# Kernel optimization log

Measured on AMD Instinct MI355X. Metric: run time of the kernel, lower is better.

The kernel has to match this reference:

```python
import jax, jax.numpy as jnp
import numpy as np

C = 64        # in_channels
E = 64        # embed_dim
K_RATIO = 0.5


def _conv(x, w, b, pad, groups):
    # x: [B,C,H,W], w: [O, I/groups, kh, kw] (torch OIHW layout)
    y = jax.lax.conv_general_dilated(
        x, w, window_strides=(1, 1), padding=[(pad, pad), (pad, pad)],
        dimension_numbers=("NCHW", "OIHW", "NCHW"), feature_group_count=groups)
    return y + b[None, :, None, None]


def setup_inputs() -> dict:
    key = jax.random.key(0)
    ks = jax.random.split(key, 16)
    s = 0.05
    return {
        "x": jax.random.normal(ks[0], (8, C, 64, 64), jnp.float32),
        "w1": jax.random.normal(ks[1], (C, C, 1, 1), jnp.float32) * s,
        "b1": jax.random.normal(ks[2], (C,), jnp.float32) * s,
        "w3": jax.random.normal(ks[3], (C, 1, 3, 3), jnp.float32) * s,
        "b3": jax.random.normal(ks[4], (C,), jnp.float32) * s,
        "w5": jax.random.normal(ks[5], (C, 1, 5, 5), jnp.float32) * s,
        "b5": jax.random.normal(ks[6], (C,), jnp.float32) * s,
        "qw": jax.random.normal(ks[7], (E, 3 * C), jnp.float32) * s,
        "qb": jax.random.normal(ks[8], (E,), jnp.float32) * s,
        "kw": jax.random.normal(ks[9], (E, 3 * C), jnp.float32) * s,
        "kb": jax.random.normal(ks[10], (E,), jnp.float32) * s,
        "vw": jax.random.normal(ks[11], (C, 3 * C), jnp.float32) * s,
        "vb": jax.random.normal(ks[12], (C,), jnp.float32) * s,
        "ow": jax.random.normal(ks[13], (C, C), jnp.float32) * s,
        "ob": jax.random.normal(ks[14], (C,), jnp.float32) * s,
    }


def reference(x, w1, b1, w3, b3, w5, b5, qw, qb, kw, kb, vw, vb, ow, ob):
    b, c, h, w = x.shape
    N = h * w
    f1 = _conv(x, w1, b1, pad=0, groups=1)        # 1x1 conv
    f2 = _conv(x, w3, b3, pad=1, groups=c)        # 3x3 depthwise
    f3 = _conv(x, w5, b5, pad=2, groups=c)        # 5x5 depthwise
    f_multi = jnp.concatenate([f1, f2, f3], axis=1)           # [b, 3c, h, w]
    f_flat = f_multi.reshape(b, 3 * c, N).transpose(0, 2, 1)  # [b, N, 3c]

    Q = jnp.einsum("bnd,ed->bne", f_flat, qw) + qb            # [b, N, E]
    K = jnp.einsum("bnd,ed->bne", f_flat, kw) + kb            # [b, N, E]
    V = jnp.einsum("bnd,cd->bnc", f_flat, vw) + vb            # [b, N, c]

    attn = jnp.einsum("bqe,bke->bqk", Q, K) / jnp.sqrt(jnp.float32(E))
    attn = jax.nn.softmax(attn, axis=-1)                      # [b, N, N]

    key_importance = attn.sum(axis=1)                         # [b, N]
    k_val = max(1, min(int(N * K_RATIO), N))
    _, topk_idx = jax.lax.top_k(key_importance, k_val)        # [b, k_val]
    mask = jnp.zeros_like(key_importance).at[
        jnp.arange(b)[:, None], topk_idx].set(1.0)            # [b, N]

    attn_c = attn * mask[:, None, :]
    attn_c = attn_c / (attn_c.sum(axis=-1, keepdims=True) + 1e-8)
    out = jnp.einsum("bqk,bkc->bqc", attn_c, V)               # [b, N, c]
    out = jnp.einsum("bnc,oc->bno", out, ow) + ob
    return out.transpose(0, 2, 1).reshape(b, c, h, w)
```

## Files before the change

kernel.cpp:

```cpp
#include <hip/hip_runtime.h>
#include <hip/hip_bf16.h>

typedef unsigned short ushort;
typedef __bf16 bf16x8 __attribute__((ext_vector_type(8)));
typedef float f32x4 __attribute__((ext_vector_type(4)));

__device__ __forceinline__ ushort f2bu(float f) {
  __hip_bfloat16 h = __float2bfloat16(f);
  return *(ushort*)&h;
}
__device__ __forceinline__ f32x4 mfma16(bf16x8 a, bf16x8 b, f32x4 c) {
  return __builtin_amdgcn_mfma_f32_16x16x32_bf16(a, b, c, 0, 0, 0);
}


__global__ __launch_bounds__(256) void k_conv(
    const float* __restrict__ x, const float* __restrict__ w1, const float* __restrict__ b1,
    const float* __restrict__ w3, const float* __restrict__ b3,
    const float* __restrict__ w5, const float* __restrict__ b5,
    ushort* __restrict__ f) {
  __shared__ float xs[64][64];
  __shared__ float w1s[64 * 65];
  __shared__ float w3s[576];
  __shared__ float w5s[1600];
  __shared__ float bs1[64], bs3[64], bs5[64];
  const int tid = threadIdx.x;
  const int y = blockIdx.x;
  const int b = blockIdx.y;
  for (int i = tid; i < 4096; i += 256) {
    int ch = i >> 6, w = i & 63;
    xs[ch][w] = x[((size_t)(b * 64 + ch) * 64 + y) * 64 + w];
  }
  for (int i = tid; i < 4096; i += 256) w1s[(i >> 6) * 65 + (i & 63)] = w1[i];
  for (int i = tid; i < 576; i += 256) w3s[i] = w3[i];
  for (int i = tid; i < 1600; i += 256) w5s[i] = w5[i];
  if (tid < 64) { bs1[tid] = b1[tid]; bs3[tid] = b3[tid]; bs5[tid] = b5[tid]; }
  __syncthreads();
  const int px = tid & 63;
  const int cg = tid >> 6;
  const int cb = cg * 16;
  ushort* fo = f + ((size_t)b * 4096 + y * 64 + px) * 192;
  float a1[16];
#pragma unroll
  for (int j = 0; j < 16; j++) a1[j] = bs1[cb + j];
  for (int ic = 0; ic < 64; ic++) {
    float xv = xs[ic][px];
#pragma unroll
    for (int j = 0; j < 16; j++) a1[j] += w1s[(cb + j) * 65 + ic] * xv;
  }
#pragma unroll
  for (int j = 0; j < 16; j++) fo[cb + j] = f2bu(a1[j]);
#pragma unroll 4
  for (int j = 0; j < 16; j++) {
    int c = cb + j;
    const float* xc = x + (size_t)(b * 64 + c) * 4096;
    float a3 = bs3[c], a5 = bs5[c];
#pragma unroll
    for (int dy = 0; dy < 5; dy++) {
      int yy = y + dy - 2;
      if (yy < 0 || yy >= 64) continue;
      const float* xr = xc + yy * 64;
#pragma unroll
      for (int dx = 0; dx < 5; dx++) {
        int wx = px + dx - 2;
        float v = (wx >= 0 && wx < 64) ? xr[wx] : 0.f;
        a5 += w5s[c * 25 + dy * 5 + dx] * v;
        if (dy >= 1 && dy <= 3 && dx >= 1 && dx <= 3)
          a3 += w3s[c * 9 + (dy - 1) * 3 + (dx - 1)] * v;
      }
    }
    fo[64 + c] = f2bu(a3);
    fo[128 + c] = f2bu(a5);
  }
}

__global__ __launch_bounds__(256) void k_w2b(
    const float* __restrict__ qw, const float* __restrict__ kw,
    const float* __restrict__ vw, ushort* __restrict__ Wb) {
  int i = blockIdx.x * 256 + threadIdx.x;
  const float* src = (i < 12288) ? qw : (i < 24576) ? kw : vw;
  int off = (i < 12288) ? i : (i < 24576) ? (i - 12288) : (i - 24576);
  Wb[i] = f2bu(src[off]);
}

__global__ __launch_bounds__(256) void k_qkv(
    const ushort* __restrict__ F, const ushort* __restrict__ Wb,
    const float* __restrict__ qb, const float* __restrict__ kb,
    const float* __restrict__ vb,
    ushort* __restrict__ Q, ushort* __restrict__ K, ushort* __restrict__ V) {
  __shared__ __align__(16) ushort fs[64][200];
  const int tid = threadIdx.x;
  const int w = tid >> 6;
  const int lane = tid & 63;
  const int col = lane & 15;
  const int quad = lane >> 4;
  const size_t rowbase = (size_t)blockIdx.x * 64;
  for (int i = tid; i < 1536; i += 256) {
    int r = i / 24, c8 = i % 24;
    *(uint4*)&fs[r][c8 * 8] = *(const uint4*)&F[rowbase * 192 + (size_t)i * 8];
  }
  __syncthreads();
  bf16x8 af[6];
#pragma unroll
  for (int kk = 0; kk < 6; kk++)
    af[kk] = *(const bf16x8*)&fs[w * 16 + col][kk * 32 + quad * 8];
  ushort* const outp[3] = {Q, K, V};
  const float* const bp[3] = {qb, kb, vb};
#pragma unroll
  for (int sel = 0; sel < 3; sel++) {
    const ushort* wsel = Wb + sel * 12288;
    const float sc = (sel == 0) ? 0.125f : 1.0f;
#pragma unroll
    for (int ntl = 0; ntl < 4; ntl++) {
      const ushort* brow = wsel + (ntl * 16 + col) * 192 + quad * 8;
      f32x4 acc = {0.f, 0.f, 0.f, 0.f};
#pragma unroll
      for (int kk = 0; kk < 6; kk++) {
        bf16x8 bf = *(const bf16x8*)&brow[kk * 32];
        acc = mfma16(af[kk], bf, acc);
      }
      float bv = bp[sel][ntl * 16 + col];
#pragma unroll
      for (int r = 0; r < 4; r++)
        outp[sel][(rowbase + w * 16 + quad * 4 + r) * 64 + ntl * 16 + col] =
            f2bu((acc[r] + bv) * sc);
    }
  }
}

__global__ __launch_bounds__(256) void k_sumexp(
    const ushort* __restrict__ Qb, const ushort* __restrict__ Kb,
    float* __restrict__ Lo, float* __restrict__ IP) {
  __shared__ float red[4][64];
  __shared__ float lred[64];
  const int tid = threadIdx.x;
  const int b = blockIdx.x & 7;
  const int qt = blockIdx.x >> 3;
  const int lane = tid & 63;
  const int w = tid >> 6;
  const int col = lane & 15;
  const int quad = lane >> 4;
  const size_t qbase = (size_t)b * 4096 + qt * 64;
  const size_t kbase = (size_t)b * 4096;
  bf16x8 af[4][2];
#pragma unroll
  for (int t = 0; t < 4; t++)
#pragma unroll
    for (int h = 0; h < 2; h++)
      af[t][h] = *(const bf16x8*)&Qb[(qbase + t * 16 + col) * 64 + quad * 8 + h * 32];
  const ushort* kp = &Kb[(kbase + w * 16 + col) * 64 + quad * 8];
  float lacc[4][4];
#pragma unroll
  for (int t = 0; t < 4; t++)
#pragma unroll
    for (int r = 0; r < 4; r++) lacc[t][r] = 0.f;
  bf16x8 nb0 = *(const bf16x8*)kp;
  bf16x8 nb1 = *(const bf16x8*)(kp + 32);
  for (int kt = 0; kt < 64; kt++) {
    bf16x8 b0 = nb0, b1 = nb1;
    if (kt < 63) {
      nb0 = *(const bf16x8*)(kp + (size_t)(kt + 1) * 4096);
      nb1 = *(const bf16x8*)(kp + (size_t)(kt + 1) * 4096 + 32);
    }
#pragma unroll
    for (int t = 0; t < 4; t++) {
      f32x4 acc = {0.f, 0.f, 0.f, 0.f};
      acc = mfma16(af[t][0], b0, acc);
      acc = mfma16(af[t][1], b1, acc);
#pragma unroll
      for (int r = 0; r < 4; r++) lacc[t][r] += __expf(acc[r]);
    }
  }
#pragma unroll
  for (int t = 0; t < 4; t++)
#pragma unroll
    for (int r = 0; r < 4; r++) {
      float v = lacc[t][r];
      v += __shfl_xor(v, 1); v += __shfl_xor(v, 2);
      v += __shfl_xor(v, 4); v += __shfl_xor(v, 8);
      if (col == 0) red[w][t * 16 + quad * 4 + r] = v;
    }
  __syncthreads();
  if (tid < 64) {
    float l = red[0][tid] + red[1][tid] + red[2][tid] + red[3][tid];
    Lo[qbase + tid] = l;
    lred[tid] = 1.f / l;
  }
  __syncthreads();
  float linv[4][4];
#pragma unroll
  for (int t = 0; t < 4; t++)
#pragma unroll
    for (int r = 0; r < 4; r++) linv[t][r] = lred[t * 16 + quad * 4 + r];
  nb0 = *(const bf16x8*)kp;
  nb1 = *(const bf16x8*)(kp + 32);
  for (int kt = 0; kt < 64; kt++) {
    bf16x8 b0 = nb0, b1 = nb1;
    if (kt < 63) {
      nb0 = *(const bf16x8*)(kp + (size_t)(kt + 1) * 4096);
      nb1 = *(const bf16x8*)(kp + (size_t)(kt + 1) * 4096 + 32);
    }
    float ip = 0.f;
#pragma unroll
    for (int t = 0; t < 4; t++) {
      f32x4 acc = {0.f, 0.f, 0.f, 0.f};
      acc = mfma16(af[t][0], b0, acc);
      acc = mfma16(af[t][1], b1, acc);
#pragma unroll
      for (int r = 0; r < 4; r++) ip += __expf(acc[r]) * linv[t][r];
    }
    ip += __shfl_xor(ip, 16);
    ip += __shfl_xor(ip, 32);
    if (quad == 0)
      IP[((size_t)(b * 64 + qt)) * 4096 + kt * 64 + w * 16 + col] = ip;
  }
}

__global__ __launch_bounds__(256) void k_impsum(
    const float* __restrict__ IP, float* __restrict__ imp) {
  const int tid = threadIdx.x;
  const int b = blockIdx.y;
  const int col = blockIdx.x * 256 + tid;
  const float* p = IP + (size_t)b * 64 * 4096 + col;
  float s = 0.f;
#pragma unroll 8
  for (int r = 0; r < 64; r++) s += p[(size_t)r * 4096];
  imp[(size_t)b * 4096 + col] = s;
}

__global__ __launch_bounds__(256) void k_mask2c(
    const float* __restrict__ imp, const ushort* __restrict__ Kb,
    const ushort* __restrict__ Vb, ushort* __restrict__ Kc,
    ushort* __restrict__ Vc) {
  __shared__ __align__(16) float imps[4096];
  __shared__ int part[4][64];
  const int tid = threadIdx.x;
  const int b = blockIdx.y;
  const int base = blockIdx.x * 64;
  for (int i = tid; i < 4096; i += 256) imps[i] = imp[(size_t)b * 4096 + i];
  __syncthreads();
  const int cand = tid & 63;
  const int seg = tid >> 6;
  const int k = base + cand;
  const float v = imps[k];
  int cnt = 0;
  const int j0 = seg * 1024;
  for (int j = j0; j < j0 + 1024; j += 4) {
    float4 a = *(const float4*)&imps[j];
    cnt += (a.x > v) ? 1 : ((a.x == v && (j + 0) < k) ? 1 : 0);
    cnt += (a.y > v) ? 1 : ((a.y == v && (j + 1) < k) ? 1 : 0);
    cnt += (a.z > v) ? 1 : ((a.z == v && (j + 2) < k) ? 1 : 0);
    cnt += (a.w > v) ? 1 : ((a.w == v && (j + 3) < k) ? 1 : 0);
  }
  part[seg][cand] = cnt;
  __syncthreads();
  const int c = part[0][cand] + part[1][cand] + part[2][cand] + part[3][cand];
  if (c < 2048) {
    const ushort* ksrc = &Kb[((size_t)b * 4096 + k) * 64 + seg * 16];
    const ushort* vsrc = &Vb[((size_t)b * 4096 + k) * 64 + seg * 16];
    ushort* kdst = &Kc[((size_t)b * 2048 + c) * 64 + seg * 16];
    ushort* vdst = &Vc[((size_t)b * 2048 + c) * 64 + seg * 16];
    *(uint4*)kdst = *(const uint4*)ksrc;
    *(uint4*)(kdst + 8) = *(const uint4*)(ksrc + 8);
    *(uint4*)vdst = *(const uint4*)vsrc;
    *(uint4*)(vdst + 8) = *(const uint4*)(vsrc + 8);
  }
}

__global__ __launch_bounds__(256) void k_attn_out(
    const ushort* __restrict__ Qb, const ushort* __restrict__ Kc,
    const ushort* __restrict__ Vc, const float* __restrict__ Lo,
    const float* __restrict__ owp, const float* __restrict__ obp,
    float* __restrict__ out) {
  __shared__ __align__(16) ushort Vt[64][72];
  __shared__ __align__(16) ushort Ps[64][72];
  __shared__ __align__(16) ushort ows[64][72];
  __shared__ float dred[4][64];
  __shared__ float lqs[64];
  const int tid = threadIdx.x;
  const int b = blockIdx.x & 7;
  const int qt = blockIdx.x >> 3;
  const int lane = tid & 63;
  const int w = tid >> 6;
  const int col = lane & 15;
  const int quad = lane >> 4;
  const size_t qbase = (size_t)b * 4096 + qt * 64;
  const size_t kbase = (size_t)b * 2048;
  bf16x8 af[4][2];
#pragma unroll
  for (int t = 0; t < 4; t++)
#pragma unroll
    for (int h = 0; h < 2; h++)
      af[t][h] = *(const bf16x8*)&Qb[(qbase + t * 16 + col) * 64 + quad * 8 + h * 32];
  for (int i = tid; i < 4096; i += 256) ows[i >> 6][i & 63] = f2bu(owp[i]);
  if (tid < 64) lqs[tid] = Lo[qbase + tid];
  f32x4 pv[4];
  float dpacc[4][4];
#pragma unroll
  for (int t = 0; t < 4; t++) {
    pv[t] = (f32x4){0.f, 0.f, 0.f, 0.f};
#pragma unroll
    for (int r = 0; r < 4; r++) dpacc[t][r] = 0.f;
  }
  const int vrow = tid & 63;
  const int vch = tid >> 6;
  const ushort* kp = &Kc[(kbase + w * 16 + col) * 64 + quad * 8];
  bf16x8 nb0 = *(const bf16x8*)kp;
  bf16x8 nb1 = *(const bf16x8*)(kp + 32);
  for (int kt = 0; kt < 32; kt++) {
    __syncthreads();
    {
      const ushort* vsrc = &Vc[(kbase + kt * 64 + vrow) * 64 + vch * 16];
      uint4 v0 = *(const uint4*)vsrc;
      uint4 v1 = *(const uint4*)(vsrc + 8);
      ushort tmp[16];
      *(uint4*)&tmp[0] = v0;
      *(uint4*)&tmp[8] = v1;
#pragma unroll
      for (int j = 0; j < 16; j++) Vt[vch * 16 + j][vrow] = tmp[j];
    }
    bf16x8 b0 = nb0, b1 = nb1;
    if (kt < 31) {
      nb0 = *(const bf16x8*)(kp + (size_t)(kt + 1) * 4096);
      nb1 = *(const bf16x8*)(kp + (size_t)(kt + 1) * 4096 + 32);
    }
#pragma unroll
    for (int t = 0; t < 4; t++) {
      f32x4 acc = {0.f, 0.f, 0.f, 0.f};
      acc = mfma16(af[t][0], b0, acc);
      acc = mfma16(af[t][1], b1, acc);
#pragma unroll
      for (int r = 0; r < 4; r++) {
        float p = __expf(acc[r]);
        dpacc[t][r] += p;
        Ps[t * 16 + quad * 4 + r][w * 16 + col] = f2bu(p);
      }
    }
    __syncthreads();
    bf16x8 v0f = *(const bf16x8*)&Vt[w * 16 + col][quad * 8];
    bf16x8 v1f = *(const bf16x8*)&Vt[w * 16 + col][quad * 8 + 32];
#pragma unroll
    for (int t = 0; t < 4; t++) {
      bf16x8 p0 = *(const bf16x8*)&Ps[t * 16 + col][quad * 8];
      bf16x8 p1 = *(const bf16x8*)&Ps[t * 16 + col][quad * 8 + 32];
      pv[t] = mfma16(p0, v0f, pv[t]);
      pv[t] = mfma16(p1, v1f, pv[t]);
    }
  }
#pragma unroll
  for (int t = 0; t < 4; t++)
#pragma unroll
    for (int r = 0; r < 4; r++) {
      float v = dpacc[t][r];
      v += __shfl_xor(v, 1); v += __shfl_xor(v, 2);
      v += __shfl_xor(v, 4); v += __shfl_xor(v, 8);
      if (col == 0) dred[w][t * 16 + quad * 4 + r] = v;
    }
  __syncthreads();
#pragma unroll
  for (int t = 0; t < 4; t++)
#pragma unroll
    for (int r = 0; r < 4; r++) {
      int q = t * 16 + quad * 4 + r;
      float den = dred[0][q] + dred[1][q] + dred[2][q] + dred[3][q] + 1e-8f * lqs[q];
      Ps[q][w * 16 + col] = f2bu(pv[t][r] / den);
    }
  __syncthreads();
  bf16x8 w0 = *(const bf16x8*)&ows[w * 16 + col][quad * 8];
  bf16x8 w1 = *(const bf16x8*)&ows[w * 16 + col][quad * 8 + 32];
  const float obv = obp[w * 16 + col];
#pragma unroll
  for (int t = 0; t < 4; t++) {
    bf16x8 p0 = *(const bf16x8*)&Ps[t * 16 + col][quad * 8];
    bf16x8 p1 = *(const bf16x8*)&Ps[t * 16 + col][quad * 8 + 32];
    f32x4 oc = {0.f, 0.f, 0.f, 0.f};
    oc = mfma16(p0, w0, oc);
    oc = mfma16(p1, w1, oc);
#pragma unroll
    for (int r = 0; r < 4; r++) {
      int q = t * 16 + quad * 4 + r;
      int co = w * 16 + col;
      out[((size_t)(b * 64 + co)) * 4096 + qt * 64 + q] = oc[r] + obv;
    }
  }
}

extern "C" void kernel_launch(void* const* d_in, const int* in_sizes, int n_in,
                              void* d_out, int out_size, void* d_ws, size_t ws_size,
                              hipStream_t stream) {
  const float* x  = (const float*)d_in[0];
  const float* w1 = (const float*)d_in[1];
  const float* b1 = (const float*)d_in[2];
  const float* w3 = (const float*)d_in[3];
  const float* b3 = (const float*)d_in[4];
  const float* w5 = (const float*)d_in[5];
  const float* b5 = (const float*)d_in[6];
  const float* qw = (const float*)d_in[7];
  const float* qb = (const float*)d_in[8];
  const float* kw = (const float*)d_in[9];
  const float* kb = (const float*)d_in[10];
  const float* vw = (const float*)d_in[11];
  const float* vb = (const float*)d_in[12];
  const float* ow = (const float*)d_in[13];
  const float* ob = (const float*)d_in[14];
  float* out = (float*)d_out;
  float* ws = (float*)d_ws;
  ushort* F   = (ushort*)ws;
  ushort* Qb  = (ushort*)(ws + 6291456);
  ushort* Kb  = (ushort*)(ws + 7340032);
  ushort* Vb  = (ushort*)(ws + 8388608);
  float*  Lo  = ws + 9437184;
  float*  IP  = ws + 9469952;
  float*  imp = ws + 11567104;
  ushort* Kc  = (ushort*)(ws + 11599872);
  ushort* Vc  = (ushort*)(ws + 12124160);
  ushort* Wb  = (ushort*)(ws + 12648448);

  k_w2b<<<144, 256, 0, stream>>>(qw, kw, vw, Wb);
  k_conv<<<dim3(64, 8), 256, 0, stream>>>(x, w1, b1, w3, b3, w5, b5, F);
  k_qkv<<<512, 256, 0, stream>>>(F, Wb, qb, kb, vb, Qb, Kb, Vb);
  k_sumexp<<<512, 256, 0, stream>>>(Qb, Kb, Lo, IP);
  k_impsum<<<dim3(16, 8), 256, 0, stream>>>(IP, imp);
  k_mask2c<<<dim3(64, 8), 256, 0, stream>>>(imp, Kb, Vb, Kc, Vc);
  k_attn_out<<<512, 256, 0, stream>>>(Qb, Kc, Vc, Lo, ow, ob, out);
}
```

Measured before the change: 327.0 us.

## Split sumexp over key halves into separate kernels and use exp2 with prescaled Q

The fused sumexp kernel becomes two kernels, each split across two key halves. That doubles the grid to 1024 blocks for more parallelism on the many CUs, and a small combine kernel merges the partial row sums and their reciprocals. Q is now prescaled by log2(e), so every exponential uses the hardware exp2 instead of __expf. The cost is two extra launches and a global round trip for the partial sums. The workspace offsets are also compacted.

```diff
diff --git a/kernel.cpp b/kernel.cpp
--- a/kernel.cpp
+++ b/kernel.cpp
@@ -12,6 +12,7 @@
 __device__ __forceinline__ f32x4 mfma16(bf16x8 a, bf16x8 b, f32x4 c) {
   return __builtin_amdgcn_mfma_f32_16x16x32_bf16(a, b, c, 0, 0, 0);
 }
+__device__ __forceinline__ float fexp2(float x) { return __builtin_amdgcn_exp2f(x); }
 
 
 __global__ __launch_bounds__(256) void k_conv(
@@ -109,7 +110,7 @@
 #pragma unroll
   for (int sel = 0; sel < 3; sel++) {
     const ushort* wsel = Wb + sel * 12288;
-    const float sc = (sel == 0) ? 0.125f : 1.0f;
+    const float sc = (sel == 0) ? 0.125f * 1.44269504088896f : 1.0f;
 #pragma unroll
     for (int ntl = 0; ntl < 4; ntl++) {
       const ushort* brow = wsel + (ntl * 16 + col) * 192 + quad * 8;
@@ -128,20 +129,21 @@
   }
 }
 
-__global__ __launch_bounds__(256) void k_sumexp(
+__global__ __launch_bounds__(256) void k_sumexp_l(
     const ushort* __restrict__ Qb, const ushort* __restrict__ Kb,
-    float* __restrict__ Lo, float* __restrict__ IP) {
+    float* __restrict__ Lp) {
   __shared__ float red[4][64];
-  __shared__ float lred[64];
   const int tid = threadIdx.x;
   const int b = blockIdx.x & 7;
-  const int qt = blockIdx.x >> 3;
+  const int rest = blockIdx.x >> 3;
+  const int qt = rest & 63;
+  const int kh = rest >> 6;
   const int lane = tid & 63;
   const int w = tid >> 6;
   const int col = lane & 15;
   const int quad = lane >> 4;
   const size_t qbase = (size_t)b * 4096 + qt * 64;
-  const size_t kbase = (size_t)b * 4096;
+  const size_t kbase = (size_t)b * 4096 + kh * 2048;
   bf16x8 af[4][2];
 #pragma unroll
   for (int t = 0; t < 4; t++)
@@ -156,9 +158,9 @@
     for (int r = 0; r < 4; r++) lacc[t][r] = 0.f;
   bf16x8 nb0 = *(const bf16x8*)kp;
   bf16x8 nb1 = *(const bf16x8*)(kp + 32);
-  for (int kt = 0; kt < 64; kt++) {
+  for (int kt = 0; kt < 32; kt++) {
     bf16x8 b0 = nb0, b1 = nb1;
-    if (kt < 63) {
+    if (kt < 31) {
       nb0 = *(const bf16x8*)(kp + (size_t)(kt + 1) * 4096);
       nb1 = *(const bf16x8*)(kp + (size_t)(kt + 1) * 4096 + 32);
     }
@@ -168,7 +170,7 @@
       acc = mfma16(af[t][0], b0, acc);
       acc = mfma16(af[t][1], b1, acc);
 #pragma unroll
-      for (int r = 0; r < 4; r++) lacc[t][r] += __expf(acc[r]);
+      for (int r = 0; r < 4; r++) lacc[t][r] += fexp2(acc[r]);
     }
   }
 #pragma unroll
@@ -183,20 +185,53 @@
   __syncthreads();
   if (tid < 64) {
     float l = red[0][tid] + red[1][tid] + red[2][tid] + red[3][tid];
-    Lo[qbase + tid] = l;
-    lred[tid] = 1.f / l;
-  }
+    Lp[((size_t)(b * 64 + qt) * 2 + kh) * 64 + tid] = l;
+  }
+}
+
+__global__ __launch_bounds__(256) void k_lcomb(
+    const float* __restrict__ Lp, float* __restrict__ Lo, float* __restrict__ Linv) {
+  int i = blockIdx.x * 256 + threadIdx.x;
+  int bqt = i >> 6, q = i & 63;
+  float l = Lp[(size_t)bqt * 128 + q] + Lp[(size_t)bqt * 128 + 64 + q];
+  Lo[i] = l;
+  Linv[i] = 1.f / l;
+}
+
+__global__ __launch_bounds__(256) void k_sumexp_ip(
+    const ushort* __restrict__ Qb, const ushort* __restrict__ Kb,
+    const float* __restrict__ Linv, float* __restrict__ IP) {
+  __shared__ float lred[64];
+  const int tid = threadIdx.x;
+  const int b = blockIdx.x & 7;
+  const int rest = blockIdx.x >> 3;
+  const int qt = rest & 63;
+  const int kh = rest >> 6;
+  const int lane = tid & 63;
+  const int w = tid >> 6;
+  const int col = lane & 15;
+  const int quad = lane >> 4;
+  const size_t qbase = (size_t)b * 4096 + qt * 64;
+  const size_t kbase = (size_t)b * 4096 + kh * 2048;
+  if (tid < 64) lred[tid] = Linv[qbase + tid];
+  bf16x8 af[4][2];
+#pragma unroll
+  for (int t = 0; t < 4; t++)
+#pragma unroll
+    for (int h = 0; h < 2; h++)
+      af[t][h] = *(const bf16x8*)&Qb[(qbase + t * 16 + col) * 64 + quad * 8 + h * 32];
   __syncthreads();
   float linv[4][4];
 #pragma unroll
   for (int t = 0; t < 4; t++)
 #pragma unroll
     for (int r = 0; r < 4; r++) linv[t][r] = lred[t * 16 + quad * 4 + r];
-  nb0 = *(const bf16x8*)kp;
-  nb1 = *(const bf16x8*)(kp + 32);
-  for (int kt = 0; kt < 64; kt++) {
+  const ushort* kp = &Kb[(kbase + w * 16 + col) * 64 + quad * 8];
+  bf16x8 nb0 = *(const bf16x8*)kp;
+  bf16x8 nb1 = *(const bf16x8*)(kp + 32);
+  for (int kt = 0; kt < 32; kt++) {
     bf16x8 b0 = nb0, b1 = nb1;
-    if (kt < 63) {
+    if (kt < 31) {
       nb0 = *(const bf16x8*)(kp + (size_t)(kt + 1) * 4096);
       nb1 = *(const bf16x8*)(kp + (size_t)(kt + 1) * 4096 + 32);
     }
@@ -207,12 +242,12 @@
       acc = mfma16(af[t][0], b0, acc);
       acc = mfma16(af[t][1], b1, acc);
 #pragma unroll
-      for (int r = 0; r < 4; r++) ip += __expf(acc[r]) * linv[t][r];
+      for (int r = 0; r < 4; r++) ip += fexp2(acc[r]) * linv[t][r];
     }
     ip += __shfl_xor(ip, 16);
     ip += __shfl_xor(ip, 32);
     if (quad == 0)
-      IP[((size_t)(b * 64 + qt)) * 4096 + kt * 64 + w * 16 + col] = ip;
+      IP[((size_t)(b * 64 + qt)) * 4096 + (kh * 32 + kt) * 64 + w * 16 + col] = ip;
   }
 }
 
@@ -331,7 +366,7 @@
       acc = mfma16(af[t][1], b1, acc);
 #pragma unroll
       for (int r = 0; r < 4; r++) {
-        float p = __expf(acc[r]);
+        float p = fexp2(acc[r]);
         dpacc[t][r] += p;
         Ps[t * 16 + quad * 4 + r][w * 16 + col] = f2bu(p);
       }
@@ -405,21 +440,25 @@
   const float* ob = (const float*)d_in[14];
   float* out = (float*)d_out;
   float* ws = (float*)d_ws;
-  ushort* F   = (ushort*)ws;
-  ushort* Qb  = (ushort*)(ws + 6291456);
-  ushort* Kb  = (ushort*)(ws + 7340032);
-  ushort* Vb  = (ushort*)(ws + 8388608);
-  float*  Lo  = ws + 9437184;
-  float*  IP  = ws + 9469952;
-  float*  imp = ws + 11567104;
-  ushort* Kc  = (ushort*)(ws + 11599872);
-  ushort* Vc  = (ushort*)(ws + 12124160);
-  ushort* Wb  = (ushort*)(ws + 12648448);
+  ushort* F    = (ushort*)ws;
+  ushort* Qb   = (ushort*)(ws + 3145728);
+  ushort* Kb   = (ushort*)(ws + 4194304);
+  ushort* Vb   = (ushort*)(ws + 5242880);
+  float*  Lo   = ws + 6291456;
+  float*  Linv = ws + 6324224;
+  float*  Lp   = ws + 6356992;
+  float*  IP   = ws + 6422528;
+  float*  imp  = ws + 8519680;
+  ushort* Kc   = (ushort*)(ws + 8552448);
+  ushort* Vc   = (ushort*)(ws + 9076736);
+  ushort* Wb   = (ushort*)(ws + 9601024);
 
   k_w2b<<<144, 256, 0, stream>>>(qw, kw, vw, Wb);
   k_conv<<<dim3(64, 8), 256, 0, stream>>>(x, w1, b1, w3, b3, w5, b5, F);
   k_qkv<<<512, 256, 0, stream>>>(F, Wb, qb, kb, vb, Qb, Kb, Vb);
-  k_sumexp<<<512, 256, 0, stream>>>(Qb, Kb, Lo, IP);
+  k_sumexp_l<<<1024, 256, 0, stream>>>(Qb, Kb, Lp);
+  k_lcomb<<<128, 256, 0, stream>>>(Lp, Lo, Linv);
+  k_sumexp_ip<<<1024, 256, 0, stream>>>(Qb, Kb, Linv, IP);
   k_impsum<<<dim3(16, 8), 256, 0, stream>>>(IP, imp);
   k_mask2c<<<dim3(64, 8), 256, 0, stream>>>(imp, Kb, Vb, Kc, Vc);
   k_attn_out<<<512, 256, 0, stream>>>(Qb, Kc, Vc, Lo, ow, ob, out);
```

Measured after the change: 356.9 us. 9.1% more time.
